# Kernel optimization log

Measured on AMD Instinct MI355X. Metric: run time of the kernel, lower is better.

Reference implementation:

```python
import jax, jax.numpy as jnp
import numpy as np
from jax import lax

NC1, NC2, NC3 = 64, 64, 512
TEMP = 1.0
EPS = 1e-5
B = 256


def setup_inputs() -> dict:
    key = jax.random.key(0)
    ks = jax.random.split(key, 16)
    d = {}
    d["inp"] = jax.random.normal(ks[0], (B, 3, 32, 32), jnp.float32)
    d["conv1_w"] = jax.random.normal(ks[1], (6, 3, 5, 5), jnp.float32) * 0.1
    d["conv1_b"] = jax.random.normal(ks[2], (6,), jnp.float32) * 0.1
    d["bn1_g"] = jnp.ones((6,), jnp.float32)
    d["bn1_b"] = jnp.zeros((6,), jnp.float32)
    d["conv2_w"] = jax.random.normal(ks[3], (16, 6, 5, 5), jnp.float32) * 0.1
    d["conv2_b"] = jax.random.normal(ks[4], (16,), jnp.float32) * 0.1
    d["bn2_g"] = jnp.ones((16,), jnp.float32)
    d["bn2_b"] = jnp.zeros((16,), jnp.float32)
    d["fc1_w"] = jax.random.normal(ks[5], (120, 400), jnp.float32) * 0.05
    d["fc1_b"] = jax.random.normal(ks[6], (120,), jnp.float32) * 0.05
    d["fc2_w"] = jax.random.normal(ks[7], (10, 120), jnp.float32) * 0.05
    d["fc2_b"] = jax.random.normal(ks[8], (10,), jnp.float32) * 0.05
    d["k1s"] = jax.random.normal(ks[9], (NC1, 6), jnp.float32)
    d["k2s"] = jax.random.normal(ks[10], (NC2, 16), jnp.float32)
    d["k3s"] = jax.random.normal(ks[11], (NC3, 120), jnp.float32)
    return d


def _conv(x, w, b):
    y = lax.conv_general_dilated(x, w, (1, 1), 'VALID',
                                 dimension_numbers=('NCHW', 'OIHW', 'NCHW'))
    return y + b[None, :, None, None]


def _bn_train(x, g, b):
    # BatchNorm2d in training mode: biased batch stats over (N,H,W)
    mean = x.mean(axis=(0, 2, 3), keepdims=True)
    var = ((x - mean) ** 2).mean(axis=(0, 2, 3), keepdims=True)
    return (x - mean) / jnp.sqrt(var + EPS) * g[None, :, None, None] + b[None, :, None, None]


def _maxpool2(x):
    return lax.reduce_window(x, -jnp.inf, lax.max, (1, 1, 2, 2), (1, 1, 2, 2), 'VALID')


def _codebook_logits_spatial(act, keys):
    # act: [B,C,H,W], keys: [K,C] -> -||act - k||_2 over C -> [B,K,H,W]
    diff = act[:, None] - keys[None, :, :, None, None]
    return -jnp.sqrt((diff ** 2).sum(axis=2))


def _neural_gas_loss(v, temp):
    n_clusters = v.shape[1]
    weightings = jnp.exp(-jnp.arange(n_clusters, dtype=v.dtype) / temp)
    sorted_v = jnp.sort(v, axis=1)
    return (sorted_v ** 2 * weightings).sum(axis=1)


def reference(inp, conv1_w, conv1_b, bn1_g, bn1_b, conv2_w, conv2_b, bn2_g, bn2_b,
              fc1_w, fc1_b, fc2_w, fc2_b, k1s, k2s, k3s):
    act1 = _bn_train(_conv(inp, conv1_w, conv1_b), bn1_g, bn1_b)          # [B,6,28,28]
    act_logits1 = _codebook_logits_spatial(act1, k1s)                     # [B,NC1,28,28]
    x = _maxpool2(jax.nn.relu(act1))                                      # [B,6,14,14]
    act2 = _bn_train(_conv(x, conv2_w, conv2_b), bn2_g, bn2_b)            # [B,16,10,10]
    act_logits2 = _codebook_logits_spatial(act2, k2s)                     # [B,NC2,10,10]
    x = _maxpool2(jax.nn.relu(act2))                                      # [B,16,5,5]
    x = x.reshape(x.shape[0], -1)                                         # [B,400]
    act3 = x @ fc1_w.T + fc1_b                                            # [B,120]
    diff3 = act3[:, None, :] - k3s[None, :, :]
    act_logits3 = -jnp.sqrt((diff3 ** 2).sum(axis=2))                     # [B,NC3]
    x = jax.nn.relu(act3)
    act4 = x @ fc2_w.T + fc2_b                                            # [B,10]
    # ARGS.ng branch: neural-gas cluster loss + argmax assignments
    cluster_loss = _neural_gas_loss(act_logits3, TEMP)                    # [B]
    assignments = jnp.argmax(act_logits3, axis=1)                         # [B] int
    return (assignments, cluster_loss.mean(), act4, act_logits1, act_logits2, act_logits3)
```

## Files before the change

kernel.cpp:

```cpp
#include <hip/hip_runtime.h>

#define B 256
#define EPSV 1e-5f

#define OFF_ASSIGN 0
#define OFF_LOSS   256
#define OFF_ACT4   257
#define OFF_L1     2817
#define OFF_L2     12847873
#define OFF_L3     14486273

__device__ __forceinline__ void wave_reduce2(float& s, float& q) {
#pragma unroll
    for (int o = 32; o > 0; o >>= 1) {
        s += __shfl_down(s, o, 64);
        q += __shfl_down(q, o, 64);
    }
}

__global__ __launch_bounds__(256) void conv1_kernel(
        const float* __restrict__ inp, const float* __restrict__ w,
        const float* __restrict__ bias, float* __restrict__ c1,
        float* __restrict__ part,
        const float* __restrict__ w1, const float* __restrict__ k3,
        float* __restrict__ w1t, float* __restrict__ k3st) {
    int bc = blockIdx.x;
    int tid = threadIdx.x;
    if (bc >= 1536) {
        int idx = (bc - 1536) * 256 + tid;
        if (idx < 48000) {
            int c = idx / 120, o = idx % 120;
            w1t[idx] = w1[o * 400 + c];
        } else if (idx < 48000 + 61440) {
            int j = idx - 48000;
            int c = j >> 9, k = j & 511;
            k3st[j] = k3[k * 120 + c];
        }
        return;
    }
    int b = bc / 6, c = bc % 6;
    __shared__ float ws[75];
    __shared__ float rs[4], rq[4];
    if (tid < 75) ws[tid] = w[c * 75 + tid];
    __syncthreads();
    const float* ip = inp + b * 3072;
    float bs = bias[c];
    float s = 0.f, sq = 0.f;
    for (int hw = tid; hw < 784; hw += 256) {
        int oh = hw / 28, ow = hw % 28;
        float acc = bs;
#pragma unroll
        for (int ic = 0; ic < 3; ++ic) {
            const float* ipc = ip + ic * 1024 + oh * 32 + ow;
            const float* wc = ws + ic * 25;
#pragma unroll
            for (int kh = 0; kh < 5; ++kh)
#pragma unroll
                for (int kw = 0; kw < 5; ++kw)
                    acc += ipc[kh * 32 + kw] * wc[kh * 5 + kw];
        }
        c1[bc * 784 + hw] = acc;
        s += acc; sq += acc * acc;
    }
    wave_reduce2(s, sq);
    if ((tid & 63) == 0) { rs[tid >> 6] = s; rq[tid >> 6] = sq; }
    __syncthreads();
    if (tid == 0) {
        part[bc * 2]     = rs[0] + rs[1] + rs[2] + rs[3];
        part[bc * 2 + 1] = rq[0] + rq[1] + rq[2] + rq[3];
    }
}

__global__ __launch_bounds__(1024) void stage1_kernel(
        const float* __restrict__ c1raw, const float* __restrict__ part1,
        const float* __restrict__ g1, const float* __restrict__ bb1,
        const float* __restrict__ k1s,
        const float* __restrict__ c2w, const float* __restrict__ c2b,
        float* __restrict__ out, float* __restrict__ c2raw,
        float* __restrict__ part2) {
    int b = blockIdx.x, tid = threadIdx.x;
    int lane = tid & 63, wid = tid >> 6;
    __shared__ __align__(16) float act[4704];
    __shared__ __align__(16) float sk1p[512];
    __shared__ float w2s[2400];
    __shared__ float xp[1176];
    __shared__ __align__(16) float sa[1600];
    __shared__ float chs[6], chq[6], ssc[6], ssh[6];
    if (wid < 6) {
        float s = 0.f, q = 0.f;
#pragma unroll
        for (int j = 0; j < 4; ++j) {
            int bi = lane + 64 * j;
            s += part1[(bi * 6 + wid) * 2];
            q += part1[(bi * 6 + wid) * 2 + 1];
        }
        wave_reduce2(s, q);
        if (lane == 0) { chs[wid] = s; chq[wid] = q; }
    }
    if (tid >= 640 && tid < 1024) {
        int idx = tid - 640;
        int k = idx / 6, c = idx - k * 6;
        sk1p[k * 8 + c] = k1s[idx];
    }
    for (int i = tid; i < 2400; i += 1024) w2s[i] = c2w[i];
    __syncthreads();
    if (tid < 6) {
        float m = chs[tid] * (1.f / 200704.f);
        float v = chq[tid] * (1.f / 200704.f) - m * m;
        float sc = g1[tid] * rsqrtf(v + EPSV);
        ssc[tid] = sc; ssh[tid] = bb1[tid] - m * sc;
    }
    if (tid >= 64 && tid < 128) {
        int k = tid - 64;
        float s = 0.f;
#pragma unroll
        for (int c = 0; c < 6; ++c) { float x = sk1p[k * 8 + c]; s += x * x; }
        sk1p[k * 8 + 6] = s;
        sk1p[k * 8 + 7] = 0.f;
    }
    __syncthreads();
    for (int i = tid; i < 4704; i += 1024) {
        int c = i / 784;
        act[i] = c1raw[b * 4704 + i] * ssc[c] + ssh[c];
    }
    __syncthreads();
    for (int i = tid; i < 1176; i += 1024) {
        int c = i / 196, p = i % 196, ph = p / 14, pw = p % 14;
        const float* ap = act + c * 784 + ph * 56 + pw * 2;
        float m = fmaxf(fmaxf(ap[0], ap[1]), fmaxf(ap[28], ap[29]));
        xp[i] = fmaxf(m, 0.f);
    }
    __syncthreads();
    if (tid < 784) {
        float a0 = act[tid], a1 = act[784 + tid], a2 = act[1568 + tid];
        float a3 = act[2352 + tid], a4 = act[3136 + tid], a5 = act[3920 + tid];
        float A2 = a0*a0 + a1*a1 + a2*a2 + a3*a3 + a4*a4 + a5*a5;
        float* op = out + OFF_L1 + (long)b * 50176 + tid;
#pragma unroll 4
        for (int k = 0; k < 64; ++k) {
            const float4* kp4 = reinterpret_cast<const float4*>(sk1p + k * 8);
            float4 kA = kp4[0], kB = kp4[1];
            float dot = a0*kA.x + a1*kA.y + a2*kA.z + a3*kA.w + a4*kB.x + a5*kB.y;
            *op = -sqrtf(fmaxf(A2 + kB.z - 2.f * dot, 0.f));
            op += 784;
        }
    } else if (tid < 944) {
        int j = tid - 784;
        int c = j / 10, oh = j - c * 10;
        float acc[10];
        float bias2 = c2b[c];
#pragma unroll
        for (int ow = 0; ow < 10; ++ow) acc[ow] = bias2;
        for (int ic = 0; ic < 6; ++ic) {
            const float* xb = xp + ic * 196;
            const float* wpc = w2s + c * 150 + ic * 25;
#pragma unroll
            for (int kh = 0; kh < 5; ++kh) {
                const float* row = xb + (oh + kh) * 14;
                float r[14];
#pragma unroll
                for (int t = 0; t < 14; ++t) r[t] = row[t];
#pragma unroll
                for (int kw = 0; kw < 5; ++kw) {
                    float wgt = wpc[kh * 5 + kw];
#pragma unroll
                    for (int ow = 0; ow < 10; ++ow)
                        acc[ow] += r[ow + kw] * wgt;
                }
            }
        }
        float* sp = sa + c * 100 + oh * 10;
        float* gp = c2raw + b * 1600 + c * 100 + oh * 10;
#pragma unroll
        for (int ow = 0; ow < 10; ++ow) { sp[ow] = acc[ow]; gp[ow] = acc[ow]; }
    }
    __syncthreads();
    {
        float s = 0.f, q = 0.f;
        if (lane < 100) { float x = sa[wid * 100 + lane]; s = x; q = x * x; }
        if (lane < 36)  { float x = sa[wid * 100 + 64 + lane]; s += x; q += x * x; }
        wave_reduce2(s, q);
        if (lane == 0) { part2[(b * 16 + wid) * 2] = s; part2[(b * 16 + wid) * 2 + 1] = q; }
    }
}

__global__ __launch_bounds__(1024) void stage2_kernel(
        const float* __restrict__ c2raw, const float* __restrict__ part2,
        const float* __restrict__ g2, const float* __restrict__ bb2,
        const float* __restrict__ k2s,
        const float* __restrict__ w1t, const float* __restrict__ f1b,
        const float* __restrict__ f2w, const float* __restrict__ f2b,
        const float* __restrict__ k3st,
        float* __restrict__ out, float* __restrict__ lossb) {
    int b = blockIdx.x >> 1, h = blockIdx.x & 1;
    int tid = threadIdx.x;
    int lane = tid & 63, wid = tid >> 6;
    __shared__ __align__(16) float sa[1600];
    __shared__ __align__(16) float sk2[1024];
    __shared__ float k2sq2[64];
    __shared__ float chs[16], chq[16], ssc[16], ssh[16];
    __shared__ float xs[400];
    __shared__ float partq[1024];
    __shared__ float a3r[120], a3p[120];
    __shared__ __align__(16) float sv[512];
    __shared__ __align__(16) float pv[1024];
    __shared__ int cntp[1024];
    __shared__ float wsum[8], wmv[8];
    __shared__ int wmi[8];
    {
        float s = 0.f, q = 0.f;
#pragma unroll
        for (int j = 0; j < 4; ++j) {
            int bi = lane + 64 * j;
            s += part2[(bi * 16 + wid) * 2];
            q += part2[(bi * 16 + wid) * 2 + 1];
        }
        wave_reduce2(s, q);
        if (lane == 0) { chs[wid] = s; chq[wid] = q; }
    }
    if (h == 0) sk2[tid] = k2s[tid];
    __syncthreads();
    if (tid < 16) {
        float m = chs[tid] * (1.f / 25600.f);
        float v = chq[tid] * (1.f / 25600.f) - m * m;
        float sc = g2[tid] * rsqrtf(v + EPSV);
        ssc[tid] = sc; ssh[tid] = bb2[tid] - m * sc;
    }
    if (h == 0 && tid >= 64 && tid < 128) {
        int k = tid - 64;
        float s = 0.f;
#pragma unroll
        for (int c = 0; c < 16; ++c) { float x = sk2[k * 16 + c]; s += x * x; }
        k2sq2[k] = s;
    }
    __syncthreads();
    for (int i = tid; i < 1600; i += 1024) {
        int c = i / 100;
        sa[i] = c2raw[b * 1600 + i] * ssc[c] + ssh[c];
    }
    __syncthreads();
    if (h == 0) {
        if (tid < 800) {
            int kg = tid / 100, hw = tid - kg * 100;
            float a[16], A2 = 0.f;
#pragma unroll
            for (int c = 0; c < 16; ++c) { a[c] = sa[c * 100 + hw]; A2 += a[c] * a[c]; }
            float* op2 = out + OFF_L2 + (long)b * 6400 + kg * 800 + hw;
#pragma unroll
            for (int k = kg * 8; k < kg * 8 + 8; ++k) {
                const float4* kp4 = reinterpret_cast<const float4*>(sk2 + k * 16);
                float4 kA = kp4[0], kB = kp4[1], kC = kp4[2], kD = kp4[3];
                float dot = a[0]*kA.x + a[1]*kA.y + a[2]*kA.z + a[3]*kA.w
                          + a[4]*kB.x + a[5]*kB.y + a[6]*kB.z + a[7]*kB.w
                          + a[8]*kC.x + a[9]*kC.y + a[10]*kC.z + a[11]*kC.w
                          + a[12]*kD.x + a[13]*kD.y + a[14]*kD.z + a[15]*kD.w;
                *op2 = -sqrtf(fmaxf(A2 + k2sq2[k] - 2.f * dot, 0.f));
                op2 += 100;
            }
        }
        return;
    }
    for (int i = tid; i < 400; i += 1024) {
        int c = i / 25, p = i % 25, ph = p / 5, pw = p % 5;
        const float* ap = sa + c * 100 + ph * 20 + pw * 2;
        float m = fmaxf(fmaxf(ap[0], ap[1]), fmaxf(ap[10], ap[11]));
        xs[i] = fmaxf(m, 0.f);
    }
    __syncthreads();
    {
        int o = tid & 127, q8 = tid >> 7;
        float s = 0.f;
        if (o < 120) {
            const float* wp = w1t + (q8 * 50) * 120 + o;
            const float2* xq = reinterpret_cast<const float2*>(xs + q8 * 50);
#pragma unroll 5
            for (int c2 = 0; c2 < 25; ++c2) {
                float2 xv = xq[c2];
                s += xv.x * wp[(2 * c2) * 120] + xv.y * wp[(2 * c2 + 1) * 120];
            }
        }
        partq[q8 * 128 + o] = s;
    }
    __syncthreads();
    if (tid < 120) {
        float acc = f1b[tid];
#pragma unroll
        for (int q8 = 0; q8 < 8; ++q8) acc += partq[q8 * 128 + tid];
        a3r[tid] = acc;
        a3p[tid] = fmaxf(acc, 0.f);
    }
    __syncthreads();
    {
        int k = tid & 511, hh = tid >> 9;
        const float* kp = k3st + k;
        float s = 0.f;
#pragma unroll 6
        for (int c = hh * 60; c < hh * 60 + 60; ++c) {
            float d = a3r[c] - kp[c * 512];
            s += d * d;
        }
        pv[hh * 512 + k] = s;
    }
    if (tid < 10) {
        float acc = f2b[tid];
        const float* wp = f2w + tid * 120;
#pragma unroll 8
        for (int c = 0; c < 120; ++c) acc += a3p[c] * wp[c];
        out[OFF_ACT4 + b * 10 + tid] = acc;
    }
    __syncthreads();
    if (tid < 512) {
        float v = -sqrtf(pv[tid] + pv[512 + tid]);
        sv[tid] = v;
        out[OFF_L3 + (long)b * 512 + tid] = v;
    }
    __syncthreads();
    {
        int i = tid & 511, hh = tid >> 9;
        float v = sv[i];
        const float4* sv4 = reinterpret_cast<const float4*>(sv);
        int cnt = 0;
#pragma unroll 8
        for (int j4 = hh * 64; j4 < hh * 64 + 64; ++j4) {
            float4 o4 = sv4[j4];
            int jb = j4 * 4;
            cnt += (o4.x < v || (o4.x == v && jb < i)) ? 1 : 0;
            cnt += (o4.y < v || (o4.y == v && jb + 1 < i)) ? 1 : 0;
            cnt += (o4.z < v || (o4.z == v && jb + 2 < i)) ? 1 : 0;
            cnt += (o4.w < v || (o4.w == v && jb + 3 < i)) ? 1 : 0;
        }
        cntp[hh * 512 + i] = cnt;
    }
    __syncthreads();
    if (tid < 512) {
        float v = sv[tid];
        int cnt = cntp[tid] + cntp[512 + tid];
        float contrib = v * v * expf(-(float)cnt);
        float ssum = contrib;
#pragma unroll
        for (int o = 32; o > 0; o >>= 1) ssum += __shfl_down(ssum, o, 64);
        float mv = v; int mi = tid;
#pragma unroll
        for (int o = 32; o > 0; o >>= 1) {
            float ov = __shfl_down(mv, o, 64);
            int oi = __shfl_down(mi, o, 64);
            if (ov > mv || (ov == mv && oi < mi)) { mv = ov; mi = oi; }
        }
        if (lane == 0) { wsum[wid] = ssum; wmv[wid] = mv; wmi[wid] = mi; }
    }
    __syncthreads();
    if (tid == 0) {
        float tot = 0.f;
        float bmv = wmv[0]; int bmi = wmi[0];
#pragma unroll
        for (int w = 0; w < 8; ++w) {
            tot += wsum[w];
            if (wmv[w] > bmv || (wmv[w] == bmv && wmi[w] < bmi)) { bmv = wmv[w]; bmi = wmi[w]; }
        }
        lossb[b] = tot;
        out[OFF_ASSIGN + b] = (float)bmi;
    }
}

__global__ void final_kernel(const float* __restrict__ loss_b, float* __restrict__ out_loss) {
    __shared__ float r[256];
    int tid = threadIdx.x;
    r[tid] = loss_b[tid];
    __syncthreads();
    for (int s = 128; s > 0; s >>= 1) {
        if (tid < s) r[tid] += r[tid + s];
        __syncthreads();
    }
    if (tid == 0) out_loss[0] = r[0] / 256.f;
}

extern "C" void kernel_launch(void* const* d_in, const int* in_sizes, int n_in,
                              void* d_out, int out_size, void* d_ws, size_t ws_size,
                              hipStream_t stream) {
    const float* inp = (const float*)d_in[0];
    const float* c1w = (const float*)d_in[1];
    const float* c1b = (const float*)d_in[2];
    const float* g1  = (const float*)d_in[3];
    const float* bb1 = (const float*)d_in[4];
    const float* c2w = (const float*)d_in[5];
    const float* c2b = (const float*)d_in[6];
    const float* g2  = (const float*)d_in[7];
    const float* bb2 = (const float*)d_in[8];
    const float* f1w = (const float*)d_in[9];
    const float* f1b = (const float*)d_in[10];
    const float* f2w = (const float*)d_in[11];
    const float* f2b = (const float*)d_in[12];
    const float* k1  = (const float*)d_in[13];
    const float* k2  = (const float*)d_in[14];
    const float* k3  = (const float*)d_in[15];
    float* out = (float*)d_out;

    float* W = (float*)d_ws;
    float* part1 = W + 64;
    float* c1raw = W + 3136;
    float* c2raw = W + 1207360;
    float* part2 = W + 1616960;
    float* lossb = W + 1625152;
    float* w1t   = W + 1625408;
    float* k3st  = W + 1673408;

    conv1_kernel<<<1964, 256, 0, stream>>>(inp, c1w, c1b, c1raw, part1,
                                           f1w, k3, w1t, k3st);
    stage1_kernel<<<B, 1024, 0, stream>>>(c1raw, part1, g1, bb1, k1, c2w, c2b,
                                          out, c2raw, part2);
    stage2_kernel<<<B * 2, 1024, 0, stream>>>(c2raw, part2, g2, bb2, k2,
                                              w1t, f1b, f2w, f2b, k3st, out, lossb);
    final_kernel<<<1, 256, 0, stream>>>(lossb, out + OFF_LOSS);
}
```

Baseline: 105.5 us.

## Hoist BN2 stats into a tiny kernel and overlay stage2 shared memory

Result: no change. 104.0 us (-1.4%).

```diff
diff --git a/kernel.cpp b/kernel.cpp
--- a/kernel.cpp
+++ b/kernel.cpp
@@ -184,10 +184,44 @@
     }
 }
 
+__global__ __launch_bounds__(512) void stats2k_kernel(
+        const float* __restrict__ part2, const float* __restrict__ g2,
+        const float* __restrict__ bb2, const float* __restrict__ k2s,
+        float* __restrict__ st2, float* __restrict__ k2sq2g) {
+    int tid = threadIdx.x;
+    __shared__ float red_s[256], red_q[256];
+    if (tid < 256) {
+        int c = tid >> 4, j = tid & 15;
+        float s = 0.f, q = 0.f;
+        for (int b = j; b < 256; b += 16) {
+            s += part2[(b * 16 + c) * 2];
+            q += part2[(b * 16 + c) * 2 + 1];
+        }
+        red_s[c * 16 + j] = s;
+        red_q[c * 16 + j] = q;
+    } else if (tid < 320) {
+        int k = tid - 256;
+        float s = 0.f;
+#pragma unroll
+        for (int c = 0; c < 16; ++c) { float x = k2s[k * 16 + c]; s += x * x; }
+        k2sq2g[k] = s;
+    }
+    __syncthreads();
+    if (tid < 16) {
+        float S = 0.f, Q = 0.f;
+#pragma unroll
+        for (int j = 0; j < 16; ++j) { S += red_s[tid * 16 + j]; Q += red_q[tid * 16 + j]; }
+        float m = S * (1.f / 25600.f);
+        float v = Q * (1.f / 25600.f) - m * m;
+        float sc = g2[tid] * rsqrtf(v + EPSV);
+        st2[tid] = sc;
+        st2[16 + tid] = bb2[tid] - m * sc;
+    }
+}
+
 __global__ __launch_bounds__(1024) void stage2_kernel(
-        const float* __restrict__ c2raw, const float* __restrict__ part2,
-        const float* __restrict__ g2, const float* __restrict__ bb2,
-        const float* __restrict__ k2s,
+        const float* __restrict__ c2raw, const float* __restrict__ st2,
+        const float* __restrict__ k2sq2g, const float* __restrict__ k2s,
         const float* __restrict__ w1t, const float* __restrict__ f1b,
         const float* __restrict__ f2w, const float* __restrict__ f2b,
         const float* __restrict__ k3st,
@@ -195,56 +229,26 @@
     int b = blockIdx.x >> 1, h = blockIdx.x & 1;
     int tid = threadIdx.x;
     int lane = tid & 63, wid = tid >> 6;
-    __shared__ __align__(16) float sa[1600];
-    __shared__ __align__(16) float sk2[1024];
-    __shared__ float k2sq2[64];
-    __shared__ float chs[16], chq[16], ssc[16], ssh[16];
-    __shared__ float xs[400];
-    __shared__ float partq[1024];
-    __shared__ float a3r[120], a3p[120];
-    __shared__ __align__(16) float sv[512];
-    __shared__ __align__(16) float pv[1024];
-    __shared__ int cntp[1024];
+    __shared__ __align__(16) float shmem[4224];
+    __shared__ float ssc[16], ssh[16];
     __shared__ float wsum[8], wmv[8];
     __shared__ int wmi[8];
-    {
-        float s = 0.f, q = 0.f;
-#pragma unroll
-        for (int j = 0; j < 4; ++j) {
-            int bi = lane + 64 * j;
-            s += part2[(bi * 16 + wid) * 2];
-            q += part2[(bi * 16 + wid) * 2 + 1];
-        }
-        wave_reduce2(s, q);
-        if (lane == 0) { chs[wid] = s; chq[wid] = q; }
-    }
-    if (h == 0) sk2[tid] = k2s[tid];
-    __syncthreads();
-    if (tid < 16) {
-        float m = chs[tid] * (1.f / 25600.f);
-        float v = chq[tid] * (1.f / 25600.f) - m * m;
-        float sc = g2[tid] * rsqrtf(v + EPSV);
-        ssc[tid] = sc; ssh[tid] = bb2[tid] - m * sc;
-    }
-    if (h == 0 && tid >= 64 && tid < 128) {
-        int k = tid - 64;
-        float s = 0.f;
-#pragma unroll
-        for (int c = 0; c < 16; ++c) { float x = sk2[k * 16 + c]; s += x * x; }
-        k2sq2[k] = s;
-    }
-    __syncthreads();
-    for (int i = tid; i < 1600; i += 1024) {
-        int c = i / 100;
-        sa[i] = c2raw[b * 1600 + i] * ssc[c] + ssh[c];
-    }
-    __syncthreads();
+    if (tid < 16) { ssc[tid] = st2[tid]; ssh[tid] = st2[16 + tid]; }
+    const float* cp = c2raw + b * 1600;
     if (h == 0) {
+        float* sk2 = shmem;
+        float* k2q = shmem + 1024;
+        sk2[tid] = k2s[tid];
+        if (tid >= 64 && tid < 128) k2q[tid - 64] = k2sq2g[tid - 64];
+        __syncthreads();
         if (tid < 800) {
             int kg = tid / 100, hw = tid - kg * 100;
             float a[16], A2 = 0.f;
 #pragma unroll
-            for (int c = 0; c < 16; ++c) { a[c] = sa[c * 100 + hw]; A2 += a[c] * a[c]; }
+            for (int c = 0; c < 16; ++c) {
+                a[c] = cp[c * 100 + hw] * ssc[c] + ssh[c];
+                A2 += a[c] * a[c];
+            }
             float* op2 = out + OFF_L2 + (long)b * 6400 + kg * 800 + hw;
 #pragma unroll
             for (int k = kg * 8; k < kg * 8 + 8; ++k) {
@@ -254,17 +258,27 @@
                           + a[4]*kB.x + a[5]*kB.y + a[6]*kB.z + a[7]*kB.w
                           + a[8]*kC.x + a[9]*kC.y + a[10]*kC.z + a[11]*kC.w
                           + a[12]*kD.x + a[13]*kD.y + a[14]*kD.z + a[15]*kD.w;
-                *op2 = -sqrtf(fmaxf(A2 + k2sq2[k] - 2.f * dot, 0.f));
+                *op2 = -sqrtf(fmaxf(A2 + k2q[k] - 2.f * dot, 0.f));
                 op2 += 100;
             }
         }
         return;
     }
+    float* xs    = shmem;
+    float* partq = shmem + 400;
+    float* a3r   = shmem + 1424;
+    float* a3p   = shmem + 1544;
+    float* sv    = shmem + 1664;
+    float* pv    = shmem + 2176;
+    int*   cntp  = (int*)(shmem + 3200);
+    __syncthreads();
     for (int i = tid; i < 400; i += 1024) {
         int c = i / 25, p = i % 25, ph = p / 5, pw = p % 5;
-        const float* ap = sa + c * 100 + ph * 20 + pw * 2;
-        float m = fmaxf(fmaxf(ap[0], ap[1]), fmaxf(ap[10], ap[11]));
-        xs[i] = fmaxf(m, 0.f);
+        const float* ap = cp + c * 100 + ph * 20 + pw * 2;
+        float sc = ssc[c], sh = ssh[c];
+        float v0 = ap[0] * sc + sh, v1 = ap[1] * sc + sh;
+        float v2 = ap[10] * sc + sh, v3 = ap[11] * sc + sh;
+        xs[i] = fmaxf(fmaxf(fmaxf(v0, v1), fmaxf(v2, v3)), 0.f);
     }
     __syncthreads();
     {
@@ -403,12 +417,15 @@
     float* lossb = W + 1625152;
     float* w1t   = W + 1625408;
     float* k3st  = W + 1673408;
+    float* st2   = W + 1734848;
+    float* k2sq  = W + 1734880;
 
     conv1_kernel<<<1964, 256, 0, stream>>>(inp, c1w, c1b, c1raw, part1,
                                            f1w, k3, w1t, k3st);
     stage1_kernel<<<B, 1024, 0, stream>>>(c1raw, part1, g1, bb1, k1, c2w, c2b,
                                           out, c2raw, part2);
-    stage2_kernel<<<B * 2, 1024, 0, stream>>>(c2raw, part2, g2, bb2, k2,
+    stats2k_kernel<<<1, 512, 0, stream>>>(part2, g2, bb2, k2, st2, k2sq);
+    stage2_kernel<<<B * 2, 1024, 0, stream>>>(c2raw, st2, k2sq, k2,
                                               w1t, f1b, f2w, f2b, k3st, out, lossb);
     final_kernel<<<1, 256, 0, stream>>>(lossb, out + OFF_LOSS);
 }
```
